# Kernel tuning notes

Hardware: AMD Instinct MI355X
Metric: run time of the kernel (lower is better)

The kernel has to match this reference:

```python
import jax, jax.numpy as jnp
import numpy as np

N, L, D, H = 16384, 50, 64, 1
N_ITEMS, N_CATS, N_RATINGS = 100000, 1000, 5


def setup_inputs() -> dict:
    key = jax.random.key(0)
    ks = jax.random.split(key, 16)
    s = 1.0 / np.sqrt(D)
    return {
        "nodes": jax.random.randint(ks[0], (N,), 0, N_ITEMS),
        "history_vc": jax.random.randint(ks[1], (N, L), 0, N_CATS),
        "history_r": jax.random.randint(ks[2], (N, L), 0, N_RATINGS),
        "c2e": jax.random.normal(ks[3], (N_CATS, D), jnp.float32),
        "v2e": jax.random.normal(ks[4], (N_ITEMS, D), jnp.float32),
        "r2e": jax.random.normal(ks[5], (N_RATINGS, D), jnp.float32),
        "W1": jax.random.normal(ks[6], (2 * D, D), jnp.float32) * s,
        "b1": jnp.zeros((D,), jnp.float32),
        "Wq": jax.random.normal(ks[7], (D, D), jnp.float32) * s,
        "bq": jnp.zeros((D,), jnp.float32),
        "Wk": jax.random.normal(ks[8], (D, D), jnp.float32) * s,
        "bk": jnp.zeros((D,), jnp.float32),
        "Wv": jax.random.normal(ks[9], (D, D), jnp.float32) * s,
        "bv": jnp.zeros((D,), jnp.float32),
        "Wo": jax.random.normal(ks[10], (D, D), jnp.float32) * s,
        "bo": jnp.zeros((D,), jnp.float32),
    }


def reference(nodes, history_vc, history_r, c2e, v2e, r2e,
              W1, b1, Wq, bq, Wk, bk, Wv, bv, Wo, bo):
    dh = D // H
    # ragged gather+concat, batched: vc=True -> categories for history, item rep for node
    e_vc = c2e[history_vc]                       # [N, L, D]
    e_r = r2e[history_r]                         # [N, L, D]
    x = jnp.concatenate([e_vc, e_r], axis=-1)    # [N, L, 2D]
    h = jax.nn.relu(jnp.einsum('nle,ed->nld', x, W1) + b1)  # [N, L, D]
    vc_rep = v2e[nodes]                          # [N, D]
    # cross-attention: single query per node over its history
    q = (vc_rep @ Wq + bq).reshape(N, H, dh)                      # [N, H, dh]
    k = (jnp.einsum('nld,de->nle', h, Wk) + bk).reshape(N, L, H, dh)
    v = (jnp.einsum('nld,de->nle', h, Wv) + bv).reshape(N, L, H, dh)
    scores = jnp.einsum('nhd,nlhd->nhl', q, k) / jnp.sqrt(jnp.float32(dh))
    attn = jax.nn.softmax(scores, axis=-1)                        # [N, H, L]
    ctx = jnp.einsum('nhl,nlhd->nhd', attn, v).reshape(N, D)      # [N, D]
    return ctx @ Wo + bo                                          # [N, D]
```

## Files before the change

kernel.cpp:

```cpp
#include <hip/hip_runtime.h>
#include <hip/hip_bf16.h>

#define LL 50
#define DD 64
#define NCATS 1000
#define NRAT 5

#define OFF_H    0
#define OFF_M1T  640000
#define OFF_WVOT 648192
#define OFF_BKQ  656384
#define OFF_BVO  656640

typedef __attribute__((ext_vector_type(8))) short short8;
typedef __attribute__((ext_vector_type(4))) float f32x4;

union U4S8 { uint4 u4; short8 s8; };

__device__ __forceinline__ float rlanef(float v, int l) {
  return __uint_as_float(__builtin_amdgcn_readlane(__float_as_uint(v), l));
}
__device__ __forceinline__ unsigned int pk2bf(float lo, float hi) {
  unsigned int r;
  asm("v_cvt_pk_bf16_f32 %0, %1, %2" : "=v"(r) : "v"(lo), "v"(hi));
  return r;
}
__device__ __forceinline__ unsigned short f2bf(float f) {
  unsigned int r;
  asm("v_cvt_pk_bf16_f32 %0, %1, %1" : "=v"(r) : "v"(f));
  return (unsigned short)r;
}
__device__ __forceinline__ short8 pack8(float4 f0, float4 f1) {
  U4S8 t;
  t.u4.x = pk2bf(f0.x, f0.y); t.u4.y = pk2bf(f0.z, f0.w);
  t.u4.z = pk2bf(f1.x, f1.y); t.u4.w = pk2bf(f1.z, f1.w);
  return t.s8;
}

__global__ __launch_bounds__(256) void prep_v3(
    const float* __restrict__ c2e, const float* __restrict__ r2e,
    const float* __restrict__ W1, const float* __restrict__ b1,
    const float* __restrict__ Wq, const float* __restrict__ bq,
    const float* __restrict__ Wk, const float* __restrict__ Wv,
    const float* __restrict__ Wo, const float* __restrict__ bv,
    const float* __restrict__ bo, char* __restrict__ ws) {
  unsigned short* H = (unsigned short*)(ws + OFF_H);
  unsigned short* M1T = (unsigned short*)(ws + OFF_M1T);
  unsigned short* WVOT = (unsigned short*)(ws + OFF_WVOT);
  float* BKQ = (float*)(ws + OFF_BKQ);
  float* BVO = (float*)(ws + OFF_BVO);

  const int tid = threadIdx.x;
  const int wid = tid >> 6;
  const int lane = tid & 63;
  const int kg = lane >> 4;
  const int rw = lane & 15;
  const int b = blockIdx.x;

  if (b < 250) {
    const int vc = __builtin_amdgcn_readfirstlane(b * 4 + wid);
    const float* __restrict__ crow = c2e + (size_t)vc * DD;
    float ac = 0.f, q0 = 0.f, q1 = 0.f, q2 = 0.f, q3 = 0.f, q4 = 0.f;
#pragma unroll 8
    for (int e = 0; e < DD; ++e) {
      const float wa = W1[(size_t)e * DD + lane];
      const float wb = W1[(size_t)(DD + e) * DD + lane];
      ac = fmaf(crow[e], wa, ac);
      q0 = fmaf(r2e[0 * DD + e], wb, q0);
      q1 = fmaf(r2e[1 * DD + e], wb, q1);
      q2 = fmaf(r2e[2 * DD + e], wb, q2);
      q3 = fmaf(r2e[3 * DD + e], wb, q3);
      q4 = fmaf(r2e[4 * DD + e], wb, q4);
    }
    const float base = ac + b1[lane];
    unsigned short* __restrict__ hrow = H + (size_t)vc * NRAT * DD + lane;
    hrow[0 * DD] = f2bf(fmaxf(base + q0, 0.f));
    hrow[1 * DD] = f2bf(fmaxf(base + q1, 0.f));
    hrow[2 * DD] = f2bf(fmaxf(base + q2, 0.f));
    hrow[3 * DD] = f2bf(fmaxf(base + q3, 0.f));
    hrow[4 * DD] = f2bf(fmaxf(base + q4, 0.f));
  } else if (b == 250) {
    short8 aq[2];
#pragma unroll
    for (int ks = 0; ks < 2; ++ks) {
      const float* __restrict__ p = Wq + (size_t)(wid * 16 + rw) * DD + ks * 32 + kg * 8;
      aq[ks] = pack8(*(const float4*)(p), *(const float4*)(p + 4));
    }
#pragma unroll
    for (int n0 = 0; n0 < 4; ++n0) {
      f32x4 a = {0.f, 0.f, 0.f, 0.f};
#pragma unroll
      for (int ks = 0; ks < 2; ++ks) {
        const float* __restrict__ p = Wk + (size_t)(n0 * 16 + rw) * DD + ks * 32 + kg * 8;
        const short8 bf = pack8(*(const float4*)(p), *(const float4*)(p + 4));
        a = __builtin_amdgcn_mfma_f32_16x16x32_bf16(aq[ks], bf, a, 0, 0, 0);
      }
#pragma unroll
      for (int r = 0; r < 4; ++r) {
        M1T[(size_t)(n0 * 16 + rw) * DD + wid * 16 + kg * 4 + r] = f2bf(a[r]);
      }
    }
    if (wid == 0) {
      const float* __restrict__ wrow = Wk + (size_t)lane * DD;
      float a0 = 0.f, a1 = 0.f, a2 = 0.f, a3 = 0.f;
#pragma unroll
      for (int t2 = 0; t2 < DD; t2 += 4) {
        const float4 w4 = *(const float4*)(wrow + t2);
        a0 = fmaf(w4.x, bq[t2 + 0], a0);
        a1 = fmaf(w4.y, bq[t2 + 1], a1);
        a2 = fmaf(w4.z, bq[t2 + 2], a2);
        a3 = fmaf(w4.w, bq[t2 + 3], a3);
      }
      BKQ[lane] = (a0 + a1) + (a2 + a3);
    }
  } else {
    short8 ao[2];
#pragma unroll
    for (int ks = 0; ks < 2; ++ks) {
      U4S8 t4;
#pragma unroll
      for (int j = 0; j < 4; ++j) {
        const int k = ks * 32 + kg * 8 + 2 * j;
        const int col = wid * 16 + rw;
        ((unsigned int*)&t4)[j] = pk2bf(Wo[(size_t)k * DD + col],
                                        Wo[(size_t)(k + 1) * DD + col]);
      }
      ao[ks] = t4.s8;
    }
#pragma unroll
    for (int n0 = 0; n0 < 4; ++n0) {
      f32x4 a = {0.f, 0.f, 0.f, 0.f};
#pragma unroll
      for (int ks = 0; ks < 2; ++ks) {
        const float* __restrict__ p = Wv + (size_t)(n0 * 16 + rw) * DD + ks * 32 + kg * 8;
        const short8 bf = pack8(*(const float4*)(p), *(const float4*)(p + 4));
        a = __builtin_amdgcn_mfma_f32_16x16x32_bf16(ao[ks], bf, a, 0, 0, 0);
      }
#pragma unroll
      for (int r = 0; r < 4; ++r) {
        WVOT[(size_t)(wid * 16 + kg * 4 + r) * DD + n0 * 16 + rw] = f2bf(a[r]);
      }
    }
    if (wid == 0) {
      float acc = bo[lane];
#pragma unroll 8
      for (int t2 = 0; t2 < DD; ++t2) acc = fmaf(bv[t2], Wo[(size_t)t2 * DD + lane], acc);
      BVO[lane] = acc;
    }
  }
}

__global__ __launch_bounds__(256, 6) void vc_main(
    const int* __restrict__ nodes, const int* __restrict__ hvc,
    const int* __restrict__ hr, const float* __restrict__ v2e,
    const char* __restrict__ ws, float* __restrict__ out, int N) {
  const unsigned short* __restrict__ H = (const unsigned short*)(ws + OFF_H);
  const unsigned short* __restrict__ M1T = (const unsigned short*)(ws + OFF_M1T);
  const unsigned short* __restrict__ WVOT = (const unsigned short*)(ws + OFF_WVOT);
  const float* __restrict__ BKQ = (const float*)(ws + OFF_BKQ);
  const float* __restrict__ BVO = (const float*)(ws + OFF_BVO);

  __shared__ __align__(16) char smem[25600 + 1088];
  char* HlB = smem;
  float* sS = (float*)(smem + 25600);

  const int tid = threadIdx.x;
  const int wid = tid >> 6;
  const int lane = tid & 63;
  const int kg = lane >> 4;
  const int rw = lane & 15;
  const int nb = blockIdx.x * 4;
  const int n = min(nb + wid, N - 1);

  const int lidx = (lane < LL) ? lane : 0;
  const int idx = hvc[(size_t)n * LL + lidx] * NRAT + hr[(size_t)n * LL + lidx];

  {
    const int chunk = lane & 7;
    char* wbase = HlB + wid * 6400;
#pragma unroll
    for (int i = 0; i < 7; ++i) {
      const int s = (i < 6) ? (i * 8 + (lane >> 3)) : (42 + (lane >> 3));
      const int sidx = __shfl(idx, s, 64);
      const char* src = (const char*)H + (size_t)sidx * 128 + ((chunk ^ (s & 7)) << 4);
      __builtin_amdgcn_global_load_lds(
          (const __attribute__((address_space(1))) void*)src,
          (__attribute__((address_space(3))) void*)(wbase + ((i < 6) ? i * 1024 : 5376)),
          16, 0, 0);
    }
  }

  {
    const int node_id = nodes[min(nb + (rw & 3), N - 1)];
    const float* __restrict__ xrow = v2e + (size_t)node_id * DD;
    short8 xa[2];
#pragma unroll
    for (int ks = 0; ks < 2; ++ks) {
      xa[ks] = pack8(*(const float4*)(xrow + ks * 32 + kg * 8),
                     *(const float4*)(xrow + ks * 32 + kg * 8 + 4));
    }
    const int n0 = wid;
    f32x4 a = {0.f, 0.f, 0.f, 0.f};
#pragma unroll
    for (int ks = 0; ks < 2; ++ks) {
      const short8 bf = *(const short8*)(M1T + (n0 * 16 + rw) * DD + ks * 32 + kg * 8);
      a = __builtin_amdgcn_mfma_f32_16x16x32_bf16(xa[ks], bf, a, 0, 0, 0);
    }
    if (kg == 0) {
      const float bkqv = BKQ[n0 * 16 + rw];
#pragma unroll
      for (int r = 0; r < 4; ++r) sS[r * 68 + n0 * 16 + rw] = a[r] + bkqv;
    }
  }
  __syncthreads();
  asm volatile("s_waitcnt vmcnt(0)" ::: "memory");
  __builtin_amdgcn_sched_barrier(0);

  const unsigned short* __restrict__ wH = (const unsigned short*)(HlB + wid * 6400);

  short8 ga[2];
#pragma unroll
  for (int ks = 0; ks < 2; ++ks) {
    const float* __restrict__ gp = sS + wid * 68 + ks * 32 + kg * 8;
    ga[ks] = pack8(*(const float4*)(gp), *(const float4*)(gp + 4));
  }
  float s0, s1, s2, s3;
  {
    f32x4 a;
#pragma unroll
    for (int lt = 0; lt < 4; ++lt) {
      const int s = lt * 16 + rw;
      a = (f32x4){0.f, 0.f, 0.f, 0.f};
#pragma unroll
      for (int ks = 0; ks < 2; ++ks) {
        const int c = (ks * 4 + kg) ^ (s & 7);
        U4S8 hb;
        hb.u4 = *(const uint4*)(wH + s * 64 + c * 8);
        a = __builtin_amdgcn_mfma_f32_16x16x32_bf16(ga[ks], hb.s8, a, 0, 0, 0);
      }
      if (lt == 0) s0 = a[0];
      else if (lt == 1) s1 = a[0];
      else if (lt == 2) s2 = a[0];
      else s3 = a[0];
    }
  }
  s0 *= 0.125f; s1 *= 0.125f; s2 *= 0.125f;
  s3 = (rw < 2) ? s3 * 0.125f : -INFINITY;

  float m = fmaxf(fmaxf(s0, s1), fmaxf(s2, s3));
#pragma unroll
  for (int x = 1; x <= 8; x <<= 1) m = fmaxf(m, __shfl_xor(m, x, 64));
  float e0 = __expf(s0 - m), e1 = __expf(s1 - m), e2 = __expf(s2 - m);
  float e3 = (rw < 2) ? __expf(s3 - m) : 0.f;
  float Z = ((e0 + e1) + (e2 + e3));
#pragma unroll
  for (int x = 1; x <= 8; x <<= 1) Z += __shfl_xor(Z, x, 64);
  const float invZ = 1.f / Z;

  {
    const int sub = (lane & 7) * 2;
    const int hi3 = lane >> 3;
    float c0 = 0.f, c1 = 0.f;
#define CTX_BLOCK(EREG, BASE, CNT, CACC)                                        \
    _Pragma("unroll")                                                           \
    for (int j = 0; j < (CNT); ++j) {                                           \
      const int l = (BASE) + j;                                                 \
      const unsigned short hbb = *(const unsigned short*)(                      \
          (const char*)wH + l * 128 + (((hi3 ^ (l & 7)) << 4) | sub));          \
      CACC = fmaf(__uint_as_float(((unsigned int)hbb) << 16),                   \
                  rlanef(EREG, j), CACC);                                       \
    }
    CTX_BLOCK(e0, 0, 16, c0)
    CTX_BLOCK(e1, 16, 16, c1)
    CTX_BLOCK(e2, 32, 16, c0)
    CTX_BLOCK(e3, 48, 2, c1)
#undef CTX_BLOCK
    sS[wid * 68 + lane] = (c0 + c1) * invZ;
  }
  __syncthreads();

  {
    short8 ca[2];
#pragma unroll
    for (int ks = 0; ks < 2; ++ks) {
      const float* __restrict__ cp = sS + (rw & 3) * 68 + ks * 32 + kg * 8;
      ca[ks] = pack8(*(const float4*)(cp), *(const float4*)(cp + 4));
    }
    const int n0 = wid;
    f32x4 a = {0.f, 0.f, 0.f, 0.f};
#pragma unroll
    for (int ks = 0; ks < 2; ++ks) {
      const short8 bf = *(const short8*)(WVOT + (n0 * 16 + rw) * DD + ks * 32 + kg * 8);
      a = __builtin_amdgcn_mfma_f32_16x16x32_bf16(ca[ks], bf, a, 0, 0, 0);
    }
    if (kg == 0) {
      const float bvov = BVO[n0 * 16 + rw];
#pragma unroll
      for (int r = 0; r < 4; ++r) {
        const int node = nb + r;
        if (node < N) out[(size_t)node * DD + n0 * 16 + rw] = a[r] + bvov;
      }
    }
  }
}

extern "C" void kernel_launch(void* const* d_in, const int* in_sizes, int n_in,
                              void* d_out, int out_size, void* d_ws, size_t ws_size,
                              hipStream_t stream) {
  const int* nodes = (const int*)d_in[0];
  const int* hvc = (const int*)d_in[1];
  const int* hr = (const int*)d_in[2];
  const float* c2e = (const float*)d_in[3];
  const float* v2e = (const float*)d_in[4];
  const float* r2e = (const float*)d_in[5];
  const float* W1 = (const float*)d_in[6];
  const float* b1 = (const float*)d_in[7];
  const float* Wq = (const float*)d_in[8];
  const float* bq = (const float*)d_in[9];
  const float* Wk = (const float*)d_in[10];
  const float* bk = (const float*)d_in[11];
  const float* Wv = (const float*)d_in[12];
  const float* bv = (const float*)d_in[13];
  const float* Wo = (const float*)d_in[14];
  const float* bo = (const float*)d_in[15];
  (void)bk;
  float* out = (float*)d_out;
  char* ws = (char*)d_ws;

  const int N = in_sizes[0];

  prep_v3<<<252, 256, 0, stream>>>(c2e, r2e, W1, b1, Wq, bq, Wk, Wv, Wo, bv, bo, ws);
  vc_main<<<(N + 3) / 4, 256, 0, stream>>>(nodes, hvc, hr, v2e, ws, out, N);
}
```

Baseline: 35.11 us.

## Process eight nodes per block with two-phase gather overlapping attention compute

Each block now handles eight nodes instead of four: each wave issues async global-to-LDS gathers for two nodes up front, then runs attention for the first node while the second node's loads are still in flight (partial vmcnt wait). The query and output projection MFMAs now use 8 of their 16 rows instead of 4, amortising the weight loads over more nodes. In exchange the block uses about twice the LDS, the launch bound drops from 6 to 3 blocks per CU, and the grid halves.

```diff
diff --git a/kernel.cpp b/kernel.cpp
--- a/kernel.cpp
+++ b/kernel.cpp
@@ -150,7 +150,7 @@
   }
 }
 
-__global__ __launch_bounds__(256, 6) void vc_main(
+__global__ __launch_bounds__(256, 3) void vc_main(
     const int* __restrict__ nodes, const int* __restrict__ hvc,
     const int* __restrict__ hr, const float* __restrict__ v2e,
     const char* __restrict__ ws, float* __restrict__ out, int N) {
@@ -160,38 +160,44 @@
   const float* __restrict__ BKQ = (const float*)(ws + OFF_BKQ);
   const float* __restrict__ BVO = (const float*)(ws + OFF_BVO);
 
-  __shared__ __align__(16) char smem[25600 + 1088];
+  __shared__ __align__(16) char smem[8 * 6400 + 8 * 68 * 4];
   char* HlB = smem;
-  float* sS = (float*)(smem + 25600);
+  float* sS = (float*)(smem + 8 * 6400);
 
   const int tid = threadIdx.x;
   const int wid = tid >> 6;
   const int lane = tid & 63;
   const int kg = lane >> 4;
   const int rw = lane & 15;
-  const int nb = blockIdx.x * 4;
-  const int n = min(nb + wid, N - 1);
+  const int nb = blockIdx.x * 8;
+  const int nA = min(nb + wid, N - 1);
+  const int nB = min(nb + 4 + wid, N - 1);
 
   const int lidx = (lane < LL) ? lane : 0;
-  const int idx = hvc[(size_t)n * LL + lidx] * NRAT + hr[(size_t)n * LL + lidx];
+  const int idxA = hvc[(size_t)nA * LL + lidx] * NRAT + hr[(size_t)nA * LL + lidx];
+  const int idxB = hvc[(size_t)nB * LL + lidx] * NRAT + hr[(size_t)nB * LL + lidx];
 
   {
     const int chunk = lane & 7;
-    char* wbase = HlB + wid * 6400;
-#pragma unroll
-    for (int i = 0; i < 7; ++i) {
-      const int s = (i < 6) ? (i * 8 + (lane >> 3)) : (42 + (lane >> 3));
-      const int sidx = __shfl(idx, s, 64);
-      const char* src = (const char*)H + (size_t)sidx * 128 + ((chunk ^ (s & 7)) << 4);
-      __builtin_amdgcn_global_load_lds(
-          (const __attribute__((address_space(1))) void*)src,
-          (__attribute__((address_space(3))) void*)(wbase + ((i < 6) ? i * 1024 : 5376)),
-          16, 0, 0);
+#pragma unroll
+    for (int ph = 0; ph < 2; ++ph) {
+      const int idx = ph ? idxB : idxA;
+      char* wbase = HlB + (ph ? (4 + wid) : wid) * 6400;
+#pragma unroll
+      for (int i = 0; i < 7; ++i) {
+        const int s = (i < 6) ? (i * 8 + (lane >> 3)) : (42 + (lane >> 3));
+        const int sidx = __shfl(idx, s, 64);
+        const char* src = (const char*)H + (size_t)sidx * 128 + ((chunk ^ (s & 7)) << 4);
+        __builtin_amdgcn_global_load_lds(
+            (const __attribute__((address_space(1))) void*)src,
+            (__attribute__((address_space(3))) void*)(wbase + ((i < 6) ? i * 1024 : 5376)),
+            16, 0, 0);
+      }
     }
   }
 
   {
-    const int node_id = nodes[min(nb + (rw & 3), N - 1)];
+    const int node_id = nodes[min(nb + (rw & 7), N - 1)];
     const float* __restrict__ xrow = v2e + (size_t)node_id * DD;
     short8 xa[2];
 #pragma unroll
@@ -206,76 +212,85 @@
       const short8 bf = *(const short8*)(M1T + (n0 * 16 + rw) * DD + ks * 32 + kg * 8);
       a = __builtin_amdgcn_mfma_f32_16x16x32_bf16(xa[ks], bf, a, 0, 0, 0);
     }
-    if (kg == 0) {
+    if (kg < 2) {
       const float bkqv = BKQ[n0 * 16 + rw];
 #pragma unroll
-      for (int r = 0; r < 4; ++r) sS[r * 68 + n0 * 16 + rw] = a[r] + bkqv;
+      for (int r = 0; r < 4; ++r) sS[(kg * 4 + r) * 68 + n0 * 16 + rw] = a[r] + bkqv;
     }
   }
   __syncthreads();
-  asm volatile("s_waitcnt vmcnt(0)" ::: "memory");
+  asm volatile("s_waitcnt vmcnt(7)" ::: "memory");
   __builtin_amdgcn_sched_barrier(0);
 
-  const unsigned short* __restrict__ wH = (const unsigned short*)(HlB + wid * 6400);
-
-  short8 ga[2];
-#pragma unroll
-  for (int ks = 0; ks < 2; ++ks) {
-    const float* __restrict__ gp = sS + wid * 68 + ks * 32 + kg * 8;
-    ga[ks] = pack8(*(const float4*)(gp), *(const float4*)(gp + 4));
-  }
-  float s0, s1, s2, s3;
-  {
-    f32x4 a;
-#pragma unroll
-    for (int lt = 0; lt < 4; ++lt) {
-      const int s = lt * 16 + rw;
-      a = (f32x4){0.f, 0.f, 0.f, 0.f};
-#pragma unroll
-      for (int ks = 0; ks < 2; ++ks) {
-        const int c = (ks * 4 + kg) ^ (s & 7);
-        U4S8 hb;
-        hb.u4 = *(const uint4*)(wH + s * 64 + c * 8);
-        a = __builtin_amdgcn_mfma_f32_16x16x32_bf16(ga[ks], hb.s8, a, 0, 0, 0);
-      }
-      if (lt == 0) s0 = a[0];
-      else if (lt == 1) s1 = a[0];
-      else if (lt == 2) s2 = a[0];
-      else s3 = a[0];
-    }
-  }
-  s0 *= 0.125f; s1 *= 0.125f; s2 *= 0.125f;
-  s3 = (rw < 2) ? s3 * 0.125f : -INFINITY;
-
-  float m = fmaxf(fmaxf(s0, s1), fmaxf(s2, s3));
-#pragma unroll
-  for (int x = 1; x <= 8; x <<= 1) m = fmaxf(m, __shfl_xor(m, x, 64));
-  float e0 = __expf(s0 - m), e1 = __expf(s1 - m), e2 = __expf(s2 - m);
-  float e3 = (rw < 2) ? __expf(s3 - m) : 0.f;
-  float Z = ((e0 + e1) + (e2 + e3));
-#pragma unroll
-  for (int x = 1; x <= 8; x <<= 1) Z += __shfl_xor(Z, x, 64);
-  const float invZ = 1.f / Z;
-
-  {
-    const int sub = (lane & 7) * 2;
-    const int hi3 = lane >> 3;
-    float c0 = 0.f, c1 = 0.f;
+#pragma unroll
+  for (int ph = 0; ph < 2; ++ph) {
+    const int myrow = ph ? (4 + wid) : wid;
+    if (ph == 1) {
+      asm volatile("s_waitcnt vmcnt(0)" ::: "memory");
+      __builtin_amdgcn_sched_barrier(0);
+    }
+    const unsigned short* __restrict__ wH =
+        (const unsigned short*)(HlB + myrow * 6400);
+
+    short8 ga[2];
+#pragma unroll
+    for (int ks = 0; ks < 2; ++ks) {
+      const float* __restrict__ gp = sS + myrow * 68 + ks * 32 + kg * 8;
+      ga[ks] = pack8(*(const float4*)(gp), *(const float4*)(gp + 4));
+    }
+    float s0, s1, s2, s3;
+    {
+      f32x4 a;
+#pragma unroll
+      for (int lt = 0; lt < 4; ++lt) {
+        const int s = lt * 16 + rw;
+        a = (f32x4){0.f, 0.f, 0.f, 0.f};
+#pragma unroll
+        for (int ks = 0; ks < 2; ++ks) {
+          const int c = (ks * 4 + kg) ^ (s & 7);
+          U4S8 hb;
+          hb.u4 = *(const uint4*)(wH + s * 64 + c * 8);
+          a = __builtin_amdgcn_mfma_f32_16x16x32_bf16(ga[ks], hb.s8, a, 0, 0, 0);
+        }
+        if (lt == 0) s0 = a[0];
+        else if (lt == 1) s1 = a[0];
+        else if (lt == 2) s2 = a[0];
+        else s3 = a[0];
+      }
+    }
+    s0 *= 0.125f; s1 *= 0.125f; s2 *= 0.125f;
+    s3 = (rw < 2) ? s3 * 0.125f : -INFINITY;
+
+    float m = fmaxf(fmaxf(s0, s1), fmaxf(s2, s3));
+#pragma unroll
+    for (int x = 1; x <= 8; x <<= 1) m = fmaxf(m, __shfl_xor(m, x, 64));
+    float e0 = __expf(s0 - m), e1 = __expf(s1 - m), e2 = __expf(s2 - m);
+    float e3 = (rw < 2) ? __expf(s3 - m) : 0.f;
+    float Z = ((e0 + e1) + (e2 + e3));
+#pragma unroll
+    for (int x = 1; x <= 8; x <<= 1) Z += __shfl_xor(Z, x, 64);
+    const float invZ = 1.f / Z;
+
+    {
+      const int sub = (lane & 7) * 2;
+      const int hi3 = lane >> 3;
+      float c0 = 0.f, c1 = 0.f;
 #define CTX_BLOCK(EREG, BASE, CNT, CACC)                                        \
-    _Pragma("unroll")                                                           \
-    for (int j = 0; j < (CNT); ++j) {                                           \
-      const int l = (BASE) + j;                                                 \
-      const unsigned short hbb = *(const unsigned short*)(                      \
-          (const char*)wH + l * 128 + (((hi3 ^ (l & 7)) << 4) | sub));          \
-      CACC = fmaf(__uint_as_float(((unsigned int)hbb) << 16),                   \
-                  rlanef(EREG, j), CACC);                                       \
-    }
-    CTX_BLOCK(e0, 0, 16, c0)
-    CTX_BLOCK(e1, 16, 16, c1)
-    CTX_BLOCK(e2, 32, 16, c0)
-    CTX_BLOCK(e3, 48, 2, c1)
+      _Pragma("unroll")                                                         \
+      for (int j = 0; j < (CNT); ++j) {                                         \
+        const int l = (BASE) + j;                                               \
+        const unsigned short hbb = *(const unsigned short*)(                    \
+            (const char*)wH + l * 128 + (((hi3 ^ (l & 7)) << 4) | sub));        \
+        CACC = fmaf(__uint_as_float(((unsigned int)hbb) << 16),                 \
+                    rlanef(EREG, j), CACC);                                     \
+      }
+      CTX_BLOCK(e0, 0, 16, c0)
+      CTX_BLOCK(e1, 16, 16, c1)
+      CTX_BLOCK(e2, 32, 16, c0)
+      CTX_BLOCK(e3, 48, 2, c1)
 #undef CTX_BLOCK
-    sS[wid * 68 + lane] = (c0 + c1) * invZ;
+      sS[myrow * 68 + lane] = (c0 + c1) * invZ;
+    }
   }
   __syncthreads();
 
@@ -283,7 +298,7 @@
     short8 ca[2];
 #pragma unroll
     for (int ks = 0; ks < 2; ++ks) {
-      const float* __restrict__ cp = sS + (rw & 3) * 68 + ks * 32 + kg * 8;
+      const float* __restrict__ cp = sS + (rw & 7) * 68 + ks * 32 + kg * 8;
       ca[ks] = pack8(*(const float4*)(cp), *(const float4*)(cp + 4));
     }
     const int n0 = wid;
@@ -293,11 +308,11 @@
       const short8 bf = *(const short8*)(WVOT + (n0 * 16 + rw) * DD + ks * 32 + kg * 8);
       a = __builtin_amdgcn_mfma_f32_16x16x32_bf16(ca[ks], bf, a, 0, 0, 0);
     }
-    if (kg == 0) {
+    if (kg < 2) {
       const float bvov = BVO[n0 * 16 + rw];
 #pragma unroll
       for (int r = 0; r < 4; ++r) {
-        const int node = nb + r;
+        const int node = nb + kg * 4 + r;
         if (node < N) out[(size_t)node * DD + n0 * 16 + rw] = a[r] + bvov;
       }
     }
@@ -330,5 +345,5 @@
   const int N = in_sizes[0];
 
   prep_v3<<<252, 256, 0, stream>>>(c2e, r2e, W1, b1, Wq, bq, Wk, Wv, Wo, bv, bo, ws);
-  vc_main<<<(N + 3) / 4, 256, 0, stream>>>(nodes, hvc, hr, v2e, ws, out, N);
-}
+  vc_main<<<(N + 7) / 8, 256, 0, stream>>>(nodes, hvc, hr, v2e, ws, out, N);
+}
```

New measurement: 32.33 us. 1.09x faster.
